# Kernel tuning notes

Hardware: AMD Instinct MI355X
Metric: run time of the kernel (lower is better)

The kernel has to match this reference:

```python
import jax, jax.numpy as jnp
import numpy as np

BS, NQ, NPTS, VOC, MAXLEN, NGT, EDIM = 16, 100, 25, 96, 25, 32, 300
ALPHA, GAMMA = 0.25, 2.0
CLASS_W, COORD_W, TEXT_W = 1.0, 1.0, 1.0
EPS_KL = 1e-6


def setup_inputs() -> dict:
    key = jax.random.key(0)
    ks = jax.random.split(key, 6)
    return {
        "pred_logits": jax.random.normal(ks[0], (BS, NQ, NPTS, 1), jnp.float32),
        "pred_ctrl_points": jax.random.uniform(ks[1], (BS, NQ, NPTS, 2), dtype=jnp.float32),
        "pred_text_logits": jax.random.normal(ks[2], (BS, NQ, NPTS, VOC + 1), jnp.float32),
        "tgt_ctrl_points": jax.random.uniform(ks[3], (BS, NGT, NPTS, 2), dtype=jnp.float32),
        "target_texts": jax.random.randint(ks[4], (BS, NGT, MAXLEN), 0, VOC + 1).astype(jnp.int32),
        "centroids": jax.random.normal(ks[5], (VOC, EDIM), jnp.float32),
    }


def reference(pred_logits, pred_ctrl_points, pred_text_logits, tgt_ctrl_points, target_texts, centroids):
    bs, nq = pred_logits.shape[:2]
    ngt = tgt_ctrl_points.shape[1]
    voc = centroids.shape[0]

    # ---- focal classification cost (per query, class 0) ----
    prob = jax.nn.sigmoid(pred_logits).reshape(bs * nq, NPTS, -1).mean(axis=1)  # (bs*nq, 1)
    neg = (1.0 - ALPHA) * prob ** GAMMA * -jnp.log(1.0 - prob + 1e-8)
    pos = ALPHA * (1.0 - prob) ** GAMMA * -jnp.log(prob + 1e-8)
    cost_class = (pos - neg)[:, 0]  # (bs*nq,)

    # ---- L1 cdist on flattened control points ----
    out_pts = pred_ctrl_points.reshape(bs * nq, -1)   # (bs*nq, npts*2)
    tgt_pts = tgt_ctrl_points.reshape(bs * ngt, -1)   # (bs*ngt, npts*2)
    cost_kpts = jnp.sum(jnp.abs(out_pts[:, None, :] - tgt_pts[None, :, :]), axis=-1)  # (bs*nq, bs*ngt)

    # ---- batched pairwise linguistic (KL) cost ----
    text_prob = jax.nn.softmax(pred_text_logits, axis=-1)[..., :voc]  # (bs,nq,npts,voc)
    pred_avg = text_prob.mean(axis=2)                                  # (bs,nq,voc)

    mask = (target_texts != voc)                 # padding index == voc
    lengths = mask.sum(axis=-1)                  # (bs,ngt)
    safe_idx = jnp.clip(target_texts, 0, voc - 1)
    # soft target per character: softmax over centroid similarities (generate_soft_target_sequence)
    sim = centroids[safe_idx] @ centroids.T / jnp.sqrt(jnp.float32(EDIM))  # (bs,ngt,maxlen,voc)
    char_dist = jax.nn.softmax(sim, axis=-1)
    tgt_avg = jnp.sum(char_dist * mask[..., None], axis=2) / jnp.maximum(lengths, 1)[..., None]  # (bs,ngt,voc)

    pred_s = jnp.maximum(pred_avg, EPS_KL)       # clamp(min=eps)
    tgt_s = jnp.maximum(tgt_avg, EPS_KL)
    tgt_s = tgt_s / tgt_s.sum(axis=-1, keepdims=True)
    logp = jnp.log(pred_s)                       # (bs,nq,voc)
    neg_ent = jnp.sum(tgt_s * jnp.log(tgt_s), axis=-1)  # (bs,ngt)
    kl = neg_ent[:, None, :] - jnp.einsum('bqc,bgc->bqg', logp, tgt_s)  # (bs,nq,ngt)
    kl = jnp.maximum(kl, 0.0)
    kl = jnp.where(lengths[:, None, :] == 0, 100.0, kl)

    # scatter per-image text cost into block-diagonal (bs*nq, bs*ngt)
    idx = jnp.arange(bs)
    cost_text = jnp.zeros((bs, nq, bs, ngt), pred_avg.dtype)
    cost_text = cost_text.at[idx, :, idx, :].set(kl)
    cost_text = cost_text.reshape(bs * nq, bs * ngt)

    C = CLASS_W * cost_class[:, None] + COORD_W * cost_kpts + TEXT_W * cost_text
    return C.reshape(bs, nq, bs * ngt)
```

## Files before the change

### kernel.cpp

```cpp
#include <hip/hip_runtime.h>
#include <math.h>

#define BS 16
#define NQ 100
#define NPTS 25
#define VOC 96
#define NC 97
#define MAXLEN 25
#define NGT 32
#define EDIM 300
#define NCOL 512
#define NDIM 50

#define WS_GRAM 0
#define WS_LOGP (WS_GRAM + NC * VOC)
#define WS_CC   (WS_LOGP + 1600 * VOC)
#define WS_TGTT (WS_CC + 1600)
#define WS_STAT (WS_TGTT + NDIM * NCOL)

#define GRAM_BLKS VOC
#define PRED_BLKS 1600
#define TR_BLKS 200
#define K1_BLKS (GRAM_BLKS + PRED_BLKS + TR_BLKS)

__global__ __launch_bounds__(128) void k1_kernel(
        const float* __restrict__ logits1,
        const float* __restrict__ tlogits,
        const float* __restrict__ cen,
        const float* __restrict__ tgt_pts,
        float* __restrict__ gram, float* __restrict__ logp,
        float* __restrict__ cost_class, float* __restrict__ tgtT) {
    __shared__ float smem[448];
    int blk = blockIdx.x, tid = threadIdx.x;
    int wave = tid >> 6, lane = tid & 63;

    if (blk < GRAM_BLKS) {
        float* row = smem;
        float* red = smem + 320;
        for (int k = tid; k < EDIM; k += 128) row[k] = cen[blk * EDIM + k];
        if (blk == 0 && tid < VOC) gram[VOC * VOC + tid] = 0.f;
        __syncthreads();
        float e = 0.f;
        if (tid < VOC) {
            float a0 = 0.f, a1 = 0.f;
            const float* c = cen + (size_t)tid * EDIM;
            for (int k = 0; k < EDIM; k += 2) { a0 += row[k] * c[k]; a1 += row[k + 1] * c[k + 1]; }
            e = __expf((a0 + a1) * 0.05773502691896258f);
        }
        red[tid] = e;
        __syncthreads();
        for (int s = 64; s; s >>= 1) { if (tid < s) red[tid] += red[tid + s]; __syncthreads(); }
        if (tid < VOC) gram[blk * VOC + tid] = e / red[0];
    } else if (blk < GRAM_BLKS + PRED_BLKS) {
        int u = blk - GRAM_BLKS;
        const float* base = tlogits + (size_t)u * NPTS * NC;
        float e0[13], e1[13], s[13], vm[13];
        int p0 = wave * 13;
#pragma unroll
        for (int i = 0; i < 13; ++i) {
            int p = p0 + i;
            bool ok = p < NPTS;
            vm[i] = ok ? 1.f : 0.f;
            int pe = ok ? p : 0;
            float x0 = base[pe * NC + lane];
            float x1 = (lane < 33) ? base[pe * NC + 64 + lane] : 0.f;
            e0[i] = __expf(x0);
            e1[i] = (lane < 33) ? __expf(x1) : 0.f;
            s[i] = e0[i] + e1[i];
        }
#pragma unroll
        for (int st = 32; st; st >>= 1) {
#pragma unroll
            for (int i = 0; i < 13; ++i) s[i] += __shfl_xor(s[i], st);
        }
        float part0 = 0.f, part1 = 0.f;
#pragma unroll
        for (int i = 0; i < 13; ++i) {
            float rinv = vm[i] / s[i];
            part0 += e0[i] * rinv;
            part1 += e1[i] * rinv;
        }
        float* pA = smem;
        pA[wave * 97 + lane] = part0;
        if (lane < 33) pA[wave * 97 + 64 + lane] = part1;
        __syncthreads();
        if (tid < VOC) {
            float tot = (pA[tid] + pA[97 + tid]) * 0.04f;
            logp[(size_t)u * VOC + tid] = __logf(fmaxf(tot, 1e-6f));
        }
        if (wave == 1) {
            float sig = 0.f;
            if (lane < NPTS) { float x = logits1[u * NPTS + lane]; sig = 1.f / (1.f + __expf(-x)); }
#pragma unroll
            for (int o = 32; o; o >>= 1) sig += __shfl_xor(sig, o);
            if (lane == 0) {
                float prob = sig * 0.04f;
                float negc = 0.75f * prob * prob * (-__logf(1.f - prob + 1e-8f));
                float posc = 0.25f * (1.f - prob) * (1.f - prob) * (-__logf(prob + 1e-8f));
                cost_class[u] = posc - negc;
            }
        }
    } else {
        int g = (blk - GRAM_BLKS - PRED_BLKS) * 128 + tid;
        int k = g / NCOL;
        int j = g - k * NCOL;
        tgtT[g] = tgt_pts[(size_t)j * NDIM + k];
    }
}

__global__ __launch_bounds__(256) void stats_kernel(
        const int*   __restrict__ texts,
        const float* __restrict__ gram,
        float* __restrict__ stat) {
    __shared__ int s_tex[4 * MAXLEN];
    int blk = blockIdx.x, tid = threadIdx.x;
    int wave = tid >> 6, lane = tid & 63;
    if (tid < 4 * MAXLEN) s_tex[tid] = texts[blk * 4 * MAXLEN + tid];
    __syncthreads();

    int vv[MAXLEN];
#pragma unroll
    for (int l = 0; l < MAXLEN; ++l) vv[l] = s_tex[wave * MAXLEN + l];
    int len = 0;
#pragma unroll
    for (int l = 0; l < MAXLEN; ++l) len += (vv[l] != VOC);
    float a0 = 0.f, a1 = 0.f;
#pragma unroll
    for (int l0 = 0; l0 < MAXLEN; l0 += 5) {
        float b0[5], b1[5];
#pragma unroll
        for (int q = 0; q < 5; ++q) {
            const float* gr = gram + vv[l0 + q] * VOC;
            b0[q] = gr[lane];
            b1[q] = (lane < 32) ? gr[64 + lane] : 0.f;
        }
#pragma unroll
        for (int q = 0; q < 5; ++q) { a0 += b0[q]; a1 += b1[q]; }
    }
    float dinv = 1.f / (float)(len > 0 ? len : 1);
    float t0 = fmaxf(a0 * dinv, 1e-6f);
    float t1 = (lane < 32) ? fmaxf(a1 * dinv, 1e-6f) : 0.f;
    float s = t0 + t1;
#pragma unroll
    for (int o = 32; o; o >>= 1) s += __shfl_xor(s, o);
    float inv = 1.f / s;
    float ts0 = t0 * inv, ts1 = t1 * inv;
    float c0 = ts0 * __logf(ts0);
    float c1 = (lane < 32) ? ts1 * __logf(ts1) : 0.f;
    float ent = c0 + c1;
#pragma unroll
    for (int o = 32; o; o >>= 1) ent += __shfl_xor(ent, o);
    float* dst = stat + (size_t)(blk * 4 + wave) * NC;
    dst[lane] = len ? ts0 : 0.f;
    if (lane < 32) dst[64 + lane] = len ? ts1 : 0.f;
    if (lane == 0) dst[VOC] = len ? ent : 100.f;
}

__global__ __launch_bounds__(256) void asm_kernel(
        const float* __restrict__ pred_pts,
        const float* __restrict__ tgtT,
        const float* __restrict__ logp,
        const float* __restrict__ cc,
        const float* __restrict__ stat,
        float* __restrict__ out) {
    __shared__ float s_lp[2][VOC];
    __shared__ float s_pp[2][NDIM];
    __shared__ float s_ct[2][NGT];
    __shared__ float spart[256];
    __shared__ float s_cc[2];

    int blk = blockIdx.x, tid = threadIdx.x;
    int pairIdx = blk >> 1, half = blk & 1;
    int r0 = pairIdx * 2;
    int b = pairIdx / 50;
    int col0 = half << 8;
    bool hasText = ((b >> 3) == half);

    if (tid < 2 * NDIM) { int r = tid >= NDIM, k = tid - r * NDIM; s_pp[r][k] = pred_pts[(size_t)(r0 + r) * NDIM + k]; }
    if (tid < 2) s_cc[tid] = cc[r0 + tid];
    if (hasText && tid >= 64 && tid < 64 + 2 * VOC) {
        int t = tid - 64;
        int r = t >= VOC, c = t - r * VOC;
        s_lp[r][c] = logp[(size_t)(r0 + r) * VOC + c];
    }
    __syncthreads();

    if (hasText) {
        {
            int pair = tid >> 2, sub = tid & 3;
            int row = pair >> 5, g = pair & 31;
            const float* L = s_lp[row] + sub * 24;
            const float* S = stat + (size_t)(b * NGT + g) * NC + sub * 24;
            float d0 = 0.f, d1 = 0.f;
#pragma unroll
            for (int j = 0; j < 24; j += 2) { d0 += L[j] * S[j]; d1 += L[j + 1] * S[j + 1]; }
            spart[tid] = d0 + d1;
        }
        __syncthreads();
        if (tid < 2 * NGT) {
            int row = tid >> 5, g = tid & 31;
            float s = spart[tid * 4] + spart[tid * 4 + 1] + spart[tid * 4 + 2] + spart[tid * 4 + 3];
            s_ct[row][g] = fmaxf(stat[(size_t)(b * NGT + g) * NC + VOC] - s, 0.f);
        }
    }

    float a0 = 0.f, a1 = 0.f;
#pragma unroll 10
    for (int k = 0; k < NDIM; ++k) {
        float tv = tgtT[(k << 9) + col0 + tid];
        a0 += fabsf(s_pp[0][k] - tv);
        a1 += fabsf(s_pp[1][k] - tv);
    }
    __syncthreads();

    int gb = tid >> 5, g = tid & 31;
    float m = (hasText && gb == (b & 7)) ? 1.f : 0.f;
    float c0v = s_cc[0], c1v = s_cc[1];
    float t0 = m * (hasText ? s_ct[0][g] : 0.f);
    float t1 = m * (hasText ? s_ct[1][g] : 0.f);
    out[(size_t)r0 * NCOL + col0 + tid]       = c0v + a0 + t0;
    out[(size_t)(r0 + 1) * NCOL + col0 + tid] = c1v + a1 + t1;
}

extern "C" void kernel_launch(void* const* d_in, const int* in_sizes, int n_in,
                              void* d_out, int out_size, void* d_ws, size_t ws_size,
                              hipStream_t stream) {
    const float* pred_logits      = (const float*)d_in[0];
    const float* pred_ctrl_points = (const float*)d_in[1];
    const float* pred_text_logits = (const float*)d_in[2];
    const float* tgt_ctrl_points  = (const float*)d_in[3];
    const int*   target_texts     = (const int*)d_in[4];
    const float* centroids        = (const float*)d_in[5];
    float* out = (float*)d_out;
    float* ws  = (float*)d_ws;

    float* gram = ws + WS_GRAM;
    float* logp = ws + WS_LOGP;
    float* cc   = ws + WS_CC;
    float* tgtT = ws + WS_TGTT;
    float* stat = ws + WS_STAT;

    k1_kernel<<<K1_BLKS, 128, 0, stream>>>(pred_logits, pred_text_logits, centroids,
                                           tgt_ctrl_points, gram, logp, cc, tgtT);
    stats_kernel<<<128, 256, 0, stream>>>(target_texts, gram, stat);
    asm_kernel<<<1600, 256, 0, stream>>>(pred_ctrl_points, tgtT, logp, cc, stat, out);
}
```

Measured before the change: 25.14 us.

## Split fused first kernel into gram, pred and transpose kernels; stage logits in LDS

Splits the combined first kernel into three separate launches (gram, per-query text softmax, target transpose). The text-softmax kernel now copies each query's logits block into shared memory with a coalesced loop, computes the softmax in place row by row, then sums columns. This replaces the 13-rows-per-wave register approach with strided global loads. It adds two kernel launches and removes the concurrency the heterogeneous blocks had inside one grid.

```diff
diff --git a/kernel.cpp b/kernel.cpp
--- a/kernel.cpp
+++ b/kernel.cpp
@@ -18,94 +18,76 @@
 #define WS_TGTT (WS_CC + 1600)
 #define WS_STAT (WS_TGTT + NDIM * NCOL)
 
-#define GRAM_BLKS VOC
-#define PRED_BLKS 1600
-#define TR_BLKS 200
-#define K1_BLKS (GRAM_BLKS + PRED_BLKS + TR_BLKS)
-
-__global__ __launch_bounds__(128) void k1_kernel(
+__global__ __launch_bounds__(128) void gram_kernel(const float* __restrict__ cen,
+                                                   float* __restrict__ gram) {
+    __shared__ float row[EDIM];
+    __shared__ float red[128];
+    int blk = blockIdx.x, tid = threadIdx.x;
+    for (int k = tid; k < EDIM; k += 128) row[k] = cen[blk * EDIM + k];
+    if (blk == 0 && tid < VOC) gram[VOC * VOC + tid] = 0.f;
+    __syncthreads();
+    float e = 0.f;
+    if (tid < VOC) {
+        float a0 = 0.f, a1 = 0.f;
+        const float* c = cen + (size_t)tid * EDIM;
+        for (int k = 0; k < EDIM; k += 2) { a0 += row[k] * c[k]; a1 += row[k + 1] * c[k + 1]; }
+        e = __expf((a0 + a1) * 0.05773502691896258f);
+    }
+    red[tid] = e;
+    __syncthreads();
+    for (int s = 64; s; s >>= 1) { if (tid < s) red[tid] += red[tid + s]; __syncthreads(); }
+    if (tid < VOC) gram[blk * VOC + tid] = e / red[0];
+}
+
+__global__ __launch_bounds__(128) void pred_kernel(
         const float* __restrict__ logits1,
         const float* __restrict__ tlogits,
-        const float* __restrict__ cen,
-        const float* __restrict__ tgt_pts,
-        float* __restrict__ gram, float* __restrict__ logp,
-        float* __restrict__ cost_class, float* __restrict__ tgtT) {
-    __shared__ float smem[448];
-    int blk = blockIdx.x, tid = threadIdx.x;
+        float* __restrict__ logp, float* __restrict__ cc) {
+    __shared__ float sm[NPTS * NC];
+    int u = blockIdx.x, tid = threadIdx.x;
     int wave = tid >> 6, lane = tid & 63;
-
-    if (blk < GRAM_BLKS) {
-        float* row = smem;
-        float* red = smem + 320;
-        for (int k = tid; k < EDIM; k += 128) row[k] = cen[blk * EDIM + k];
-        if (blk == 0 && tid < VOC) gram[VOC * VOC + tid] = 0.f;
-        __syncthreads();
-        float e = 0.f;
-        if (tid < VOC) {
-            float a0 = 0.f, a1 = 0.f;
-            const float* c = cen + (size_t)tid * EDIM;
-            for (int k = 0; k < EDIM; k += 2) { a0 += row[k] * c[k]; a1 += row[k + 1] * c[k + 1]; }
-            e = __expf((a0 + a1) * 0.05773502691896258f);
-        }
-        red[tid] = e;
-        __syncthreads();
-        for (int s = 64; s; s >>= 1) { if (tid < s) red[tid] += red[tid + s]; __syncthreads(); }
-        if (tid < VOC) gram[blk * VOC + tid] = e / red[0];
-    } else if (blk < GRAM_BLKS + PRED_BLKS) {
-        int u = blk - GRAM_BLKS;
-        const float* base = tlogits + (size_t)u * NPTS * NC;
-        float e0[13], e1[13], s[13], vm[13];
-        int p0 = wave * 13;
-#pragma unroll
-        for (int i = 0; i < 13; ++i) {
-            int p = p0 + i;
-            bool ok = p < NPTS;
-            vm[i] = ok ? 1.f : 0.f;
-            int pe = ok ? p : 0;
-            float x0 = base[pe * NC + lane];
-            float x1 = (lane < 33) ? base[pe * NC + 64 + lane] : 0.f;
-            e0[i] = __expf(x0);
-            e1[i] = (lane < 33) ? __expf(x1) : 0.f;
-            s[i] = e0[i] + e1[i];
-        }
-#pragma unroll
-        for (int st = 32; st; st >>= 1) {
-#pragma unroll
-            for (int i = 0; i < 13; ++i) s[i] += __shfl_xor(s[i], st);
-        }
-        float part0 = 0.f, part1 = 0.f;
-#pragma unroll
-        for (int i = 0; i < 13; ++i) {
-            float rinv = vm[i] / s[i];
-            part0 += e0[i] * rinv;
-            part1 += e1[i] * rinv;
-        }
-        float* pA = smem;
-        pA[wave * 97 + lane] = part0;
-        if (lane < 33) pA[wave * 97 + 64 + lane] = part1;
-        __syncthreads();
-        if (tid < VOC) {
-            float tot = (pA[tid] + pA[97 + tid]) * 0.04f;
-            logp[(size_t)u * VOC + tid] = __logf(fmaxf(tot, 1e-6f));
-        }
-        if (wave == 1) {
-            float sig = 0.f;
-            if (lane < NPTS) { float x = logits1[u * NPTS + lane]; sig = 1.f / (1.f + __expf(-x)); }
-#pragma unroll
-            for (int o = 32; o; o >>= 1) sig += __shfl_xor(sig, o);
-            if (lane == 0) {
-                float prob = sig * 0.04f;
-                float negc = 0.75f * prob * prob * (-__logf(1.f - prob + 1e-8f));
-                float posc = 0.25f * (1.f - prob) * (1.f - prob) * (-__logf(prob + 1e-8f));
-                cost_class[u] = posc - negc;
-            }
-        }
-    } else {
-        int g = (blk - GRAM_BLKS - PRED_BLKS) * 128 + tid;
-        int k = g / NCOL;
-        int j = g - k * NCOL;
-        tgtT[g] = tgt_pts[(size_t)j * NDIM + k];
-    }
+    const float* src = tlogits + (size_t)u * NPTS * NC;
+    for (int i = tid; i < NPTS * NC; i += 128) sm[i] = src[i];
+    __syncthreads();
+    for (int p = wave; p < NPTS; p += 2) {
+        float* r = sm + p * NC;
+        float x0 = r[lane];
+        float x1 = (lane < 33) ? r[64 + lane] : 0.f;
+        float e0 = __expf(x0);
+        float e1 = (lane < 33) ? __expf(x1) : 0.f;
+        float s = e0 + e1;
+#pragma unroll
+        for (int o = 32; o; o >>= 1) s += __shfl_xor(s, o);
+        float inv = 1.f / s;
+        r[lane] = e0 * inv;
+        if (lane < 33) r[64 + lane] = e1 * inv;
+    }
+    __syncthreads();
+    if (tid < VOC) {
+        float acc = 0.f;
+#pragma unroll
+        for (int p = 0; p < NPTS; ++p) acc += sm[p * NC + tid];
+        logp[(size_t)u * VOC + tid] = __logf(fmaxf(acc * 0.04f, 1e-6f));
+    }
+    if (wave == 1) {
+        float sig = 0.f;
+        if (lane < NPTS) { float x = logits1[u * NPTS + lane]; sig = 1.f / (1.f + __expf(-x)); }
+#pragma unroll
+        for (int o = 32; o; o >>= 1) sig += __shfl_xor(sig, o);
+        if (lane == 0) {
+            float prob = sig * 0.04f;
+            float negc = 0.75f * prob * prob * (-__logf(1.f - prob + 1e-8f));
+            float posc = 0.25f * (1.f - prob) * (1.f - prob) * (-__logf(prob + 1e-8f));
+            cc[u] = posc - negc;
+        }
+    }
+}
+
+__global__ __launch_bounds__(256) void tr_kernel(const float* __restrict__ tgt_pts,
+                                                 float* __restrict__ tgtT) {
+    int gidx = blockIdx.x * 256 + threadIdx.x;
+    int k = gidx >> 9, j = gidx & 511;
+    tgtT[gidx] = tgt_pts[(size_t)j * NDIM + k];
 }
 
 __global__ __launch_bounds__(256) void stats_kernel(
@@ -240,8 +222,9 @@
     float* tgtT = ws + WS_TGTT;
     float* stat = ws + WS_STAT;
 
-    k1_kernel<<<K1_BLKS, 128, 0, stream>>>(pred_logits, pred_text_logits, centroids,
-                                           tgt_ctrl_points, gram, logp, cc, tgtT);
+    gram_kernel<<<VOC, 128, 0, stream>>>(centroids, gram);
+    pred_kernel<<<1600, 128, 0, stream>>>(pred_logits, pred_text_logits, logp, cc);
+    tr_kernel<<<100, 256, 0, stream>>>(tgt_ctrl_points, tgtT);
     stats_kernel<<<128, 256, 0, stream>>>(target_texts, gram, stat);
     asm_kernel<<<1600, 256, 0, stream>>>(pred_ctrl_points, tgtT, logp, cc, stat, out);
 }
```

New measurement: 31.84 us, median of 2. 26.6% more time.
